# Kernel optimization log

Hardware: AMD Instinct MI355X
Metric: run time of the kernel (lower is better)

The kernel has to match this reference:

```python
import jax, jax.numpy as jnp
import numpy as np

B, L, DIN, D, H, NL, NE, TOPK, DFF, NOUT = 128, 128, 6, 256, 8, 6, 8, 2, 1024, 5
NMOE = NL // 2
DK = D // H
EPS = 1e-5


def setup_inputs() -> dict:
    key = jax.random.key(0)
    ks = iter(jax.random.split(key, 32))
    s = 0.02
    rn = lambda shape, scale=s: jax.random.normal(next(ks), shape, dtype=jnp.float32) * scale
    return {
        "x": jax.random.normal(next(ks), (B, L, DIN), dtype=jnp.float32),
        "emb_w": rn((DIN, D)), "emb_b": jnp.zeros((D,), jnp.float32),
        # wave attention layers (stacked over NL)
        "wq": rn((NL, D, D)), "wk": rn((NL, D, D)), "wv": rn((NL, D, D)), "wo": rn((NL, D, D)),
        "wfreq": rn((NL, H), 0.1), "wphase": jnp.zeros((NL, H), jnp.float32),
        # MoE layers (stacked over NMOE, experts over NE)
        "rtw": rn((NMOE, D, NE)), "rtb": jnp.zeros((NMOE, NE), jnp.float32),
        "ew1": rn((NMOE, NE, D, DFF)), "eb1": jnp.zeros((NMOE, NE, DFF), jnp.float32),
        "ew2": rn((NMOE, NE, DFF, D)), "eb2": jnp.zeros((NMOE, NE, D), jnp.float32),
        "ln_g": jnp.ones((D,), jnp.float32), "ln_b": jnp.zeros((D,), jnp.float32),
        "pred_w": rn((D, NOUT)), "pred_b": jnp.zeros((NOUT,), jnp.float32),
        "unc_w": rn((D, NOUT)), "unc_b": jnp.zeros((NOUT,), jnp.float32),
    }


def _wave_attn(x, Wq, Wk, Wv, Wo, freq, phase):
    # x: (B, L, D)
    q = (x @ Wq).reshape(B, L, H, DK).transpose(0, 2, 1, 3)  # (B,H,L,DK)
    k = (x @ Wk).reshape(B, L, H, DK).transpose(0, 2, 1, 3)
    v = (x @ Wv).reshape(B, L, H, DK).transpose(0, 2, 1, 3)
    pos = jnp.arange(L, dtype=x.dtype)
    wave = jnp.cos(2.0 * np.pi * freq[:, None] * pos[None, :] + phase[:, None])  # (H,L)
    scores = jnp.einsum("bhqd,bhkd->bhqk", q, k) * (DK ** -0.5)
    scores = scores * wave[None, :, None, :]  # modulate along key axis
    attn = jax.nn.softmax(scores, axis=-1)
    out = jnp.einsum("bhqk,bhkd->bhqd", attn, v)
    out = out.transpose(0, 2, 1, 3).reshape(B, L, D)
    return out @ Wo


def _moe(x, rw, rb, w1, b1, w2, b2):
    # x: (B, L, D). Dense per-expert compute + top-k combine weights
    xf = x.reshape(-1, D)  # (T, D), T = B*L
    T = xf.shape[0]
    p = jax.nn.softmax(xf @ rw + rb, axis=-1)           # (T, NE)
    tw, ti = jax.lax.top_k(p, TOPK)                      # (T, TOPK)
    tw = tw / tw.sum(axis=-1, keepdims=True)
    comb = jnp.zeros((T, NE), xf.dtype).at[jnp.arange(T)[:, None], ti].add(tw)  # (T, NE)
    h = jax.nn.gelu(jnp.einsum("td,edf->etf", xf, w1) + b1[:, None, :], approximate=False)
    eo = jnp.einsum("etf,efd->etd", h, w2) + b2[:, None, :]  # (NE, T, D)
    out = jnp.einsum("te,etd->td", comb, eo)
    return out.reshape(B, L, D)


def _forward(x, emb_w, emb_b, wq, wk, wv, wo, wfreq, wphase,
             rtw, rtb, ew1, eb1, ew2, eb2, ln_g, ln_b,
             pred_w, pred_b, unc_w, unc_b):
    h = x @ emb_w + emb_b
    for i in range(NL):
        h = _wave_attn(h, wq[i], wk[i], wv[i], wo[i], wfreq[i], wphase[i]) + h
        if i % 2 == 0 and i // 2 < NMOE:
            m = i // 2
            h = _moe(h, rtw[m], rtb[m], ew1[m], eb1[m], ew2[m], eb2[m]) + h
    mu = h.mean(axis=-1, keepdims=True)
    var = ((h - mu) ** 2).mean(axis=-1, keepdims=True)
    h = (h - mu) * jax.lax.rsqrt(var + EPS) * ln_g + ln_b
    latent = h[:, -1, :]  # (B, D)
    pred = latent @ pred_w + pred_b
    uncertainty = jax.nn.softplus(latent @ unc_w + unc_b)
    return pred, uncertainty


def reference(x, emb_w, emb_b, wq, wk, wv, wo, wfreq, wphase,
              rtw, rtb, ew1, eb1, ew2, eb2, ln_g, ln_b,
              pred_w, pred_b, unc_w, unc_b):
    return _forward(x, emb_w, emb_b, wq, wk, wv, wo, wfreq, wphase,
                    rtw, rtb, ew1, eb1, ew2, eb2, ln_g, ln_b,
                    pred_w, pred_b, unc_w, unc_b)
```

## Files before the change

### kernel.cpp

```cpp
#include <hip/hip_runtime.h>
#include <hip/hip_bf16.h>
#include <math.h>

#define B_    128
#define L_    128
#define DIN   6
#define D_    256
#define H_    8
#define NL_   6
#define NE_   8
#define DFF_  1024
#define NOUT_ 5
#define T_    (B_*L_)
#define DK_   32
#define NDESC_MAX 264

typedef unsigned short u16;
typedef __hip_bfloat16 bf16;
typedef __attribute__((ext_vector_type(8))) short short8;
typedef __attribute__((ext_vector_type(8))) unsigned short ushort8v;
typedef __attribute__((ext_vector_type(4))) float floatx4;

__device__ const int S_PRE[16] = {
    0, 98304, 99840, 100096, 100144, 100192, 106336, 106360,
    130936, 137080, 137336, 137592, 138872, 138877, 140157, 140162};
__device__ const int S_SRC[15] = {0,1,2,7,8,9,10,12,14,15,16,17,18,19,20};
#define NSMALL 140162

struct SrcPtrs { const void* p[21]; };

__device__ __forceinline__ float bf2f(u16 u) {
    return __uint_as_float(((unsigned)u) << 16);
}
__device__ __forceinline__ u16 f2bf(float f) {
    union { bf16 b; u16 u; } c; c.b = __float2bfloat16(f); return c.u;
}
__device__ __forceinline__ float gelu_f(float x) {
    return 0.5f * x * (1.0f + erff(x * 0.70710678118654752f));
}

__global__ __launch_bounds__(256)
void conv_small_kernel(SrcPtrs P, float* __restrict__ dst)
{
    const int i = blockIdx.x * 256 + threadIdx.x;
    if (i >= NSMALL) return;
    int seg = 0;
    #pragma unroll
    for (int s = 1; s < 15; ++s) seg += (i >= S_PRE[s]) ? 1 : 0;
    const int off = i - S_PRE[seg];
    const void* src = P.p[S_SRC[seg]];
    const bool isbf = (((const u16*)P.p[15])[0] == 0x3F80);
    if (isbf) dst[i] = bf2f(((const u16*)src)[off]);
    else      dst[i] = ((const float*)src)[off];
}

template<int KD, int ND>
__global__ __launch_bounds__(256)
void transpose_kernel(const void* __restrict__ src, const u16* __restrict__ probe,
                      u16* __restrict__ dst, long dzs, int noff, int total)
{
    const int i = blockIdx.x * 256 + threadIdx.x;
    if (i >= total) return;
    const int z   = i / (KD * ND);
    const int rem = i - z * (KD * ND);
    const int n   = rem / KD;
    const int k   = rem - n * KD;
    const size_t si = (size_t)z * KD * ND + (size_t)k * ND + n;
    const bool isbf = (probe[0] == 0x3F80);
    const float v = isbf ? bf2f(((const u16*)src)[si]) : ((const float*)src)[si];
    dst[(size_t)z * dzs + (size_t)(n + noff) * KD + k] = f2bf(v);
}

__global__ __launch_bounds__(256)
void embed_kernel(const float* __restrict__ x, const float* __restrict__ emb_w,
                  const float* __restrict__ emb_b, float* __restrict__ h,
                  u16* __restrict__ hb)
{
    const int idx = blockIdx.x * 256 + threadIdx.x;
    const int t = idx >> 8;
    const int d = idx & 255;
    float acc = emb_b[d];
    #pragma unroll
    for (int j = 0; j < DIN; ++j)
        acc += x[t * DIN + j] * emb_w[j * D_ + d];
    h[idx]  = acc;
    hb[idx] = f2bf(acc);
}

template<int EPI, int MODE>
__global__ __launch_bounds__(256)
void mfma_gemm(const u16* __restrict__ A, int lda, int K,
               const u16* __restrict__ Wt, long wzs, int ldwt,
               const float* __restrict__ biasb, long bzs,
               void* __restrict__ CoutV, int ldc,
               u16* __restrict__ hbout, int Mfixed,
               const int* __restrict__ cnt, const int* __restrict__ base_,
               const int* __restrict__ atok,
               const int* __restrict__ de, const int* __restrict__ dr,
               const int* __restrict__ ndesc)
{
    int M, r0, sbase = 0, e = 0;
    if constexpr (MODE == 0) {
        M  = Mfixed;
        r0 = blockIdx.x * 128;
        if (r0 >= M) return;
    } else {
        const int i = blockIdx.x;
        if (i >= *ndesc) return;
        e     = de[i];
        r0    = dr[i] * 128;
        sbase = base_[e];
        M     = cnt[e];
    }
    const u16*   W    = Wt + (size_t)e * wzs;
    const float* bias = biasb ? (biasb + (size_t)e * bzs) : nullptr;
    const int col0 = blockIdx.y * 128;

    __shared__ __attribute__((aligned(16))) u16 As[2][128][40];
    __shared__ __attribute__((aligned(16))) u16 Bs[2][128][40];
    __shared__ int stok[128];

    const int tid  = threadIdx.x;
    const int lane = tid & 63;
    const int wave = tid >> 6;
    const int wm = wave & 1, wn = wave >> 1;

    if constexpr (MODE == 1) {
        if (tid < 128) {
            int rr = r0 + tid;
            if (rr >= M) rr = M - 1;
            stok[tid] = atok[sbase + rr];
        }
        __syncthreads();
    }

    const int srow = tid >> 1;
    const int sk   = (tid & 1) * 16;
    long arow;
    if constexpr (MODE == 1) {
        arow = stok[srow];
    } else {
        int rr = r0 + srow;
        if (rr >= M) rr = M - 1;
        arow = (MODE == 2) ? (long)(sbase + rr) : (long)rr;
    }
    const u16* ga = A + arow * (long)lda + sk;
    const u16* gw = W + (size_t)(col0 + srow) * ldwt + sk;

    floatx4 acc[4][4];
    #pragma unroll
    for (int i = 0; i < 4; ++i)
        #pragma unroll
        for (int j = 0; j < 4; ++j)
            acc[i][j] = (floatx4){0.f, 0.f, 0.f, 0.f};

    const int fm = wm * 64 + (lane & 15);
    const int fn = wn * 64 + (lane & 15);
    const int fk = (lane >> 4) * 8;

    ushort8v ra0 = *(const ushort8v*)(ga);
    ushort8v ra1 = *(const ushort8v*)(ga + 8);
    ushort8v rb0 = *(const ushort8v*)(gw);
    ushort8v rb1 = *(const ushort8v*)(gw + 8);

    const int nt = K >> 5;
    int buf = 0;
    for (int t = 0; t < nt; ++t) {
        *(ushort8v*)&As[buf][srow][sk]     = ra0;
        *(ushort8v*)&As[buf][srow][sk + 8] = ra1;
        *(ushort8v*)&Bs[buf][srow][sk]     = rb0;
        *(ushort8v*)&Bs[buf][srow][sk + 8] = rb1;
        __syncthreads();

        if (t + 1 < nt) {
            const int k0 = (t + 1) << 5;
            ra0 = *(const ushort8v*)(ga + k0);
            ra1 = *(const ushort8v*)(ga + k0 + 8);
            rb0 = *(const ushort8v*)(gw + k0);
            rb1 = *(const ushort8v*)(gw + k0 + 8);
        }

        short8 af[4], bfr[4];
        #pragma unroll
        for (int i = 0; i < 4; ++i) af[i]  = *(const short8*)&As[buf][fm + 16*i][fk];
        #pragma unroll
        for (int j = 0; j < 4; ++j) bfr[j] = *(const short8*)&Bs[buf][fn + 16*j][fk];
        #pragma unroll
        for (int i = 0; i < 4; ++i)
            #pragma unroll
            for (int j = 0; j < 4; ++j)
                acc[i][j] = __builtin_amdgcn_mfma_f32_16x16x32_bf16(
                    af[i], bfr[j], acc[i][j], 0, 0, 0);
        buf ^= 1;
    }

    const int er = wm * 64 + ((lane >> 4) << 2);
    const int ec = wn * 64 + (lane & 15);
    #pragma unroll
    for (int i = 0; i < 4; ++i) {
        #pragma unroll
        for (int reg = 0; reg < 4; ++reg) {
            const int lrow = r0 + er + i * 16 + reg;
            if (lrow >= M) continue;
            const long crow = (MODE == 0) ? (long)lrow : (long)(sbase + lrow);
            #pragma unroll
            for (int j = 0; j < 4; ++j) {
                const int cj = col0 + ec + j * 16;
                const float val = acc[i][j][reg];
                if constexpr (EPI == 0) {
                    ((u16*)CoutV)[crow * ldc + cj] = f2bf(val);
                } else if constexpr (EPI == 1) {
                    const size_t idx = crow * ldc + cj;
                    const float nv = ((float*)CoutV)[idx] + val;
                    ((float*)CoutV)[idx] = nv;
                    hbout[idx] = f2bf(nv);
                } else if constexpr (EPI == 2) {
                    ((u16*)CoutV)[crow * ldc + cj] = f2bf(gelu_f(val + bias[cj]));
                } else {
                    ((float*)CoutV)[crow * ldc + cj] = val + bias[cj];
                }
            }
        }
    }
}

__global__ __launch_bounds__(256)
void attn_kernel(const u16* __restrict__ qkv, u16* __restrict__ o,
                 const float* __restrict__ wfreq, const float* __restrict__ wphase)
{
    const int bh = blockIdx.x;
    const int b  = bh >> 3;
    const int hh = bh & 7;

    __shared__ __attribute__((aligned(16))) u16 Qs[128][40];
    __shared__ __attribute__((aligned(16))) u16 Ks[128][40];
    __shared__ __attribute__((aligned(16))) u16 Vt[32][136];
    __shared__ __attribute__((aligned(16))) u16 Ps[128][136];
    __shared__ float wavec[128];

    const int tid  = threadIdx.x;
    const int lane = tid & 63;
    const int w    = tid >> 6;
    const int col16 = lane & 15;
    const int quad  = lane >> 4;

    const long qbase = (long)b * L_ * 768 + hh * DK_;

    {
        const int row = tid >> 1;
        const int hf  = (tid & 1) * 16;
        const u16* src = qkv + qbase + (long)row * 768 + hf;
        *(ushort8v*)&Qs[row][hf]     = *(const ushort8v*)(src);
        *(ushort8v*)&Qs[row][hf + 8] = *(const ushort8v*)(src + 8);
        *(ushort8v*)&Ks[row][hf]     = *(const ushort8v*)(src + 256);
        *(ushort8v*)&Ks[row][hf + 8] = *(const ushort8v*)(src + 264);
        #pragma unroll
        for (int j = 0; j < 16; ++j)
            Vt[hf + j][row] = src[512 + j];
    }
    if (tid < L_) {
        float f2 = 6.2831853071795864769f * wfreq[hh];
        wavec[tid] = cosf(f2 * (float)tid + wphase[hh]);
    }
    __syncthreads();

    const float scale = 0.17677669529663687f;
    float wv8[8];
    #pragma unroll
    for (int ni = 0; ni < 8; ++ni)
        wv8[ni] = scale * wavec[ni * 16 + col16];

    const int m0 = w * 32;
    floatx4 accs[2][8];
    {
        short8 a0 = *(const short8*)&Qs[m0 + col16][quad * 8];
        short8 a1 = *(const short8*)&Qs[m0 + 16 + col16][quad * 8];
        #pragma unroll
        for (int ni = 0; ni < 8; ++ni) {
            short8 bf = *(const short8*)&Ks[ni * 16 + col16][quad * 8];
            accs[0][ni] = __builtin_amdgcn_mfma_f32_16x16x32_bf16(
                a0, bf, (floatx4){0.f,0.f,0.f,0.f}, 0, 0, 0);
            accs[1][ni] = __builtin_amdgcn_mfma_f32_16x16x32_bf16(
                a1, bf, (floatx4){0.f,0.f,0.f,0.f}, 0, 0, 0);
        }
    }
    #pragma unroll
    for (int mi = 0; mi < 2; ++mi)
        #pragma unroll
        for (int ni = 0; ni < 8; ++ni)
            #pragma unroll
            for (int reg = 0; reg < 4; ++reg)
                accs[mi][ni][reg] *= wv8[ni];

    #pragma unroll
    for (int mi = 0; mi < 2; ++mi) {
        #pragma unroll
        for (int reg = 0; reg < 4; ++reg) {
            float rmax = -1e30f;
            #pragma unroll
            for (int ni = 0; ni < 8; ++ni)
                rmax = fmaxf(rmax, accs[mi][ni][reg]);
            #pragma unroll
            for (int off = 1; off < 16; off <<= 1)
                rmax = fmaxf(rmax, __shfl_xor(rmax, off));
            float e[8], rsum = 0.0f;
            #pragma unroll
            for (int ni = 0; ni < 8; ++ni) {
                e[ni] = expf(accs[mi][ni][reg] - rmax);
                rsum += e[ni];
            }
            #pragma unroll
            for (int off = 1; off < 16; off <<= 1)
                rsum += __shfl_xor(rsum, off);
            const float inv = 1.0f / rsum;
            const int row = m0 + mi * 16 + quad * 4 + reg;
            #pragma unroll
            for (int ni = 0; ni < 8; ++ni)
                Ps[row][ni * 16 + col16] = f2bf(e[ni] * inv);
        }
    }
    __syncthreads();

    floatx4 acco[2][2];
    #pragma unroll
    for (int mi = 0; mi < 2; ++mi)
        #pragma unroll
        for (int nj = 0; nj < 2; ++nj)
            acco[mi][nj] = (floatx4){0.f,0.f,0.f,0.f};
    #pragma unroll
    for (int kk = 0; kk < 4; ++kk) {
        short8 a0 = *(const short8*)&Ps[m0 + col16][kk * 32 + quad * 8];
        short8 a1 = *(const short8*)&Ps[m0 + 16 + col16][kk * 32 + quad * 8];
        short8 b0 = *(const short8*)&Vt[col16][kk * 32 + quad * 8];
        short8 b1 = *(const short8*)&Vt[16 + col16][kk * 32 + quad * 8];
        acco[0][0] = __builtin_amdgcn_mfma_f32_16x16x32_bf16(a0, b0, acco[0][0], 0, 0, 0);
        acco[0][1] = __builtin_amdgcn_mfma_f32_16x16x32_bf16(a0, b1, acco[0][1], 0, 0, 0);
        acco[1][0] = __builtin_amdgcn_mfma_f32_16x16x32_bf16(a1, b0, acco[1][0], 0, 0, 0);
        acco[1][1] = __builtin_amdgcn_mfma_f32_16x16x32_bf16(a1, b1, acco[1][1], 0, 0, 0);
    }

    const long obase = (long)b * L_ * D_ + hh * DK_;
    #pragma unroll
    for (int mi = 0; mi < 2; ++mi)
        #pragma unroll
        for (int reg = 0; reg < 4; ++reg) {
            const int row = m0 + mi * 16 + quad * 4 + reg;
            #pragma unroll
            for (int nj = 0; nj < 2; ++nj)
                o[obase + (long)row * D_ + nj * 16 + col16] =
                    f2bf(acco[mi][nj][reg]);
        }
}

__global__ __launch_bounds__(256)
void router_kernel(const float* __restrict__ h, const float* __restrict__ rtw,
                   const float* __restrict__ rtb, int* __restrict__ te,
                   float* __restrict__ twt)
{
    const int tid  = threadIdx.x;
    const int lane = tid & 63;
    const int wv   = tid >> 6;
    const int t    = blockIdx.x * 4 + wv;

    const float4 hv = ((const float4*)(h + (long)t * D_))[lane];
    const float4* rp = (const float4*)rtw;

    float lg[NE_];
    #pragma unroll
    for (int e = 0; e < NE_; ++e) lg[e] = 0.0f;
    #pragma unroll
    for (int i = 0; i < 4; ++i) {
        const int d = lane * 4 + i;
        const float xv = (i == 0) ? hv.x : (i == 1) ? hv.y : (i == 2) ? hv.z : hv.w;
        float4 wa = rp[d * 2 + 0];
        float4 wb = rp[d * 2 + 1];
        lg[0] = fmaf(xv, wa.x, lg[0]);
        lg[1] = fmaf(xv, wa.y, lg[1]);
        lg[2] = fmaf(xv, wa.z, lg[2]);
        lg[3] = fmaf(xv, wa.w, lg[3]);
        lg[4] = fmaf(xv, wb.x, lg[4]);
        lg[5] = fmaf(xv, wb.y, lg[5]);
        lg[6] = fmaf(xv, wb.z, lg[6]);
        lg[7] = fmaf(xv, wb.w, lg[7]);
    }
    #pragma unroll
    for (int off = 1; off < 64; off <<= 1)
        #pragma unroll
        for (int e = 0; e < NE_; ++e)
            lg[e] += __shfl_xor(lg[e], off);

    if (lane == 0) {
        #pragma unroll
        for (int e = 0; e < NE_; ++e) lg[e] += rtb[e];
        int i1 = 0; float v1 = lg[0];
        #pragma unroll
        for (int e = 1; e < NE_; ++e) { if (lg[e] > v1) { v1 = lg[e]; i1 = e; } }
        int i2 = (i1 == 0) ? 1 : 0; float v2 = lg[i2];
        #pragma unroll
        for (int e = 0; e < NE_; ++e) {
            if (e != i1 && lg[e] > v2) { v2 = lg[e]; i2 = e; }
        }
        float r   = expf(v2 - v1);
        float wa1 = 1.0f / (1.0f + r);
        te[2 * t]     = i1;
        te[2 * t + 1] = i2;
        twt[2 * t]     = wa1;
        twt[2 * t + 1] = r * wa1;
    }
}

__global__ __launch_bounds__(512)
void countscan_kernel(const int* __restrict__ te, int* __restrict__ cnt,
                      int* __restrict__ base_, int* __restrict__ cursor,
                      int* __restrict__ de, int* __restrict__ dr,
                      int* __restrict__ ndesc)
{
    const int tid = threadIdx.x;
    int c[NE_];
    #pragma unroll
    for (int e = 0; e < NE_; ++e) c[e] = 0;
    for (int i = tid; i < 2 * T_; i += 512) {
        const int e = te[i];
        #pragma unroll
        for (int ee = 0; ee < NE_; ++ee) c[ee] += (e == ee) ? 1 : 0;
    }
    #pragma unroll
    for (int off = 1; off < 64; off <<= 1)
        #pragma unroll
        for (int e = 0; e < NE_; ++e)
            c[e] += __shfl_xor(c[e], off);

    __shared__ int wsum[8][NE_];
    const int lane = tid & 63, wv = tid >> 6;
    if (lane == 0)
        #pragma unroll
        for (int e = 0; e < NE_; ++e) wsum[wv][e] = c[e];
    __syncthreads();
    if (tid == 0) {
        int a = 0, n = 0;
        for (int e = 0; e < NE_; ++e) {
            int s = 0;
            for (int w = 0; w < 8; ++w) s += wsum[w][e];
            cnt[e] = s;
            base_[e] = a;
            a += s;
            const int nb = (s + 127) >> 7;
            for (int rb = 0; rb < nb; ++rb) {
                de[n] = e; dr[n] = rb; ++n;
            }
        }
        *ndesc = n;
    }
    if (tid < NE_) cursor[tid] = 0;
}

__global__ __launch_bounds__(256)
void scatter_kernel(const int* __restrict__ te, const int* __restrict__ base_,
                    int* __restrict__ cursor, int* __restrict__ atok,
                    int* __restrict__ tslot)
{
    __shared__ int lcnt[NE_];
    __shared__ int gb[NE_];
    const int tid = threadIdx.x;
    if (tid < NE_) lcnt[tid] = 0;
    __syncthreads();

    const int i0 = blockIdx.x * 512 + tid * 2;
    const int e0 = te[i0], e1 = te[i0 + 1];
    const int r0 = atomicAdd(&lcnt[e0], 1);
    const int r1 = atomicAdd(&lcnt[e1], 1);
    __syncthreads();
    if (tid < NE_) gb[tid] = atomicAdd(&cursor[tid], lcnt[tid]);
    __syncthreads();

    const int s0 = base_[e0] + gb[e0] + r0;
    const int s1 = base_[e1] + gb[e1] + r1;
    atok[s0] = i0 >> 1;
    atok[s1] = i0 >> 1;
    tslot[i0]     = s0;
    tslot[i0 + 1] = s1;
}

__global__ __launch_bounds__(256)
void combine_kernel(float* __restrict__ h, u16* __restrict__ hb,
                    const float* __restrict__ eo,
                    const float* __restrict__ twt, const int* __restrict__ tslot)
{
    const int t = blockIdx.x;
    const int d = threadIdx.x;
    const int s0 = tslot[2 * t], s1 = tslot[2 * t + 1];
    const float w0 = twt[2 * t], w1 = twt[2 * t + 1];
    const long idx = (long)t * D_ + d;
    const float nv = h[idx] + w0 * eo[(long)s0 * D_ + d] + w1 * eo[(long)s1 * D_ + d];
    h[idx]  = nv;
    hb[idx] = f2bf(nv);
}

__global__ __launch_bounds__(256)
void final_kernel(const float* __restrict__ h, const float* __restrict__ ln_g,
                  const float* __restrict__ ln_b, const float* __restrict__ pred_w,
                  const float* __restrict__ pred_b, const float* __restrict__ unc_w,
                  const float* __restrict__ unc_b, float* __restrict__ out)
{
    const int b = blockIdx.x;
    const int d = threadIdx.x;
    const long t = (long)b * L_ + (L_ - 1);
    const float val = h[t * D_ + d];

    __shared__ float red[4];
    __shared__ float lat[D_];

    float s = val;
    #pragma unroll
    for (int off = 32; off > 0; off >>= 1) s += __shfl_down(s, off);
    if ((d & 63) == 0) red[d >> 6] = s;
    __syncthreads();
    const float mean = (red[0] + red[1] + red[2] + red[3]) * (1.0f / D_);
    __syncthreads();

    const float dv = val - mean;
    s = dv * dv;
    #pragma unroll
    for (int off = 32; off > 0; off >>= 1) s += __shfl_down(s, off);
    if ((d & 63) == 0) red[d >> 6] = s;
    __syncthreads();
    const float var = (red[0] + red[1] + red[2] + red[3]) * (1.0f / D_);

    lat[d] = dv * rsqrtf(var + 1e-5f) * ln_g[d] + ln_b[d];
    __syncthreads();

    if (d < 2 * NOUT_) {
        const int j = d % NOUT_;
        const int sel = d / NOUT_;
        const float* w  = sel ? unc_w : pred_w;
        const float* bb = sel ? unc_b : pred_b;
        float acc = bb[j];
        for (int dd = 0; dd < D_; ++dd)
            acc = fmaf(lat[dd], w[dd * NOUT_ + j], acc);
        if (sel) acc = log1pf(expf(acc));
        out[sel * (B_ * NOUT_) + b * NOUT_ + j] = acc;
    }
}

extern "C" void kernel_launch(void* const* d_in, const int* in_sizes, int n_in,
                              void* d_out, int out_size, void* d_ws, size_t ws_size,
                              hipStream_t stream)
{
    (void)in_sizes; (void)n_in; (void)out_size; (void)ws_size;

    char* ws = (char*)d_ws;
    size_t off = 0;
    auto alloc = [&](size_t bytes) {
        size_t cur = off;
        off += (bytes + 255) & ~(size_t)255;
        return (void*)(ws + cur);
    };
    float* cs     = (float*)alloc((size_t)NSMALL * 4);
    u16*   qkvt   = (u16*)  alloc((size_t)NL_ * 768 * 256 * 2);
    u16*   wot    = (u16*)  alloc((size_t)NL_ * 256 * 256 * 2);
    u16*   ew1t   = (u16*)  alloc((size_t)3 * NE_ * DFF_ * D_ * 2);
    u16*   ew2t   = (u16*)  alloc((size_t)3 * NE_ * D_ * DFF_ * 2);
    float* h      = (float*)alloc((size_t)T_ * D_ * 4);
    u16*   hb     = (u16*)  alloc((size_t)T_ * D_ * 2);
    char*  uni    = (char*) alloc((size_t)2 * T_ * DFF_ * 2 + (size_t)2 * T_ * D_ * 4);
    u16*   qkvb   = (u16*)  uni;
    u16*   ob     = (u16*)  (uni + (size_t)T_ * 768 * 2 + 256);
    u16*   hidden = (u16*)  uni;
    float* eo     = (float*)(uni + (size_t)2 * T_ * DFF_ * 2);
    int*   te     = (int*)  alloc((size_t)2 * T_ * 4);
    float* twt    = (float*)alloc((size_t)2 * T_ * 4);
    int*   atok   = (int*)  alloc((size_t)2 * T_ * 4);
    int*   tslot  = (int*)  alloc((size_t)2 * T_ * 4);
    int*   cnt    = (int*)  alloc(64 * 4);
    int*   base_  = (int*)  alloc(64 * 4);
    int*   cursor = (int*)  alloc(64 * 4);
    int*   de     = (int*)  alloc(NDESC_MAX * 4);
    int*   dr     = (int*)  alloc(NDESC_MAX * 4);
    int*   ndesc  = (int*)  alloc(64 * 4);

    SrcPtrs P;
    for (int i = 0; i < 21; ++i) P.p[i] = d_in[i];
    const u16* probe = (const u16*)d_in[15];

    conv_small_kernel<<<(NSMALL + 255) / 256, 256, 0, stream>>>(P, cs);
    transpose_kernel<256,256><<<(NL_*65536 + 255)/256, 256, 0, stream>>>(
        d_in[3], probe, qkvt, 768L*256, 0,   NL_*65536);
    transpose_kernel<256,256><<<(NL_*65536 + 255)/256, 256, 0, stream>>>(
        d_in[4], probe, qkvt, 768L*256, 256, NL_*65536);
    transpose_kernel<256,256><<<(NL_*65536 + 255)/256, 256, 0, stream>>>(
        d_in[5], probe, qkvt, 768L*256, 512, NL_*65536);
    transpose_kernel<256,256><<<(NL_*65536 + 255)/256, 256, 0, stream>>>(
        d_in[6], probe, wot, 65536L, 0, NL_*65536);
    transpose_kernel<256,1024><<<(24*262144 + 255)/256, 256, 0, stream>>>(
        d_in[11], probe, ew1t, 262144L, 0, 24*262144);
    transpose_kernel<1024,256><<<(24*262144 + 255)/256, 256, 0, stream>>>(
        d_in[13], probe, ew2t, 262144L, 0, 24*262144);

    const float* x      = cs;
    const float* emb_w  = cs + 98304;
    const float* emb_b  = cs + 99840;
    const float* wfreq  = cs + 100096;
    const float* wphase = cs + 100144;
    const float* rtw    = cs + 100192;
    const float* rtb    = cs + 106336;
    const float* eb1    = cs + 106360;
    const float* eb2    = cs + 130936;
    const float* ln_g   = cs + 137080;
    const float* ln_b   = cs + 137336;
    const float* pred_w = cs + 137592;
    const float* pred_b = cs + 138872;
    const float* unc_w  = cs + 138877;
    const float* unc_b  = cs + 140157;

    embed_kernel<<<(T_ * D_) / 256, 256, 0, stream>>>(x, emb_w, emb_b, h, hb);

    for (int i = 0; i < NL_; ++i) {
        mfma_gemm<0, 0><<<dim3(T_/128, 6, 1), 256, 0, stream>>>(
            hb, D_, D_, qkvt + (size_t)i * 768 * 256, 0, 256,
            nullptr, 0, qkvb, 768, nullptr, T_,
            nullptr, nullptr, nullptr, nullptr, nullptr, nullptr);
        attn_kernel<<<B_ * H_, 256, 0, stream>>>(qkvb, ob,
                                                 wfreq + i * H_, wphase + i * H_);
        mfma_gemm<1, 0><<<dim3(T_/128, 2, 1), 256, 0, stream>>>(
            ob, D_, D_, wot + (size_t)i * 65536, 0, 256,
            nullptr, 0, h, D_, hb, T_,
            nullptr, nullptr, nullptr, nullptr, nullptr, nullptr);

        if (i % 2 == 0) {
            const int m = i / 2;
            const u16* w1t = ew1t + (size_t)m * NE_ * DFF_ * D_;
            const u16* w2t = ew2t + (size_t)m * NE_ * D_ * DFF_;
            const float* b1 = eb1 + (size_t)m * NE_ * DFF_;
            const float* b2 = eb2 + (size_t)m * NE_ * D_;
            router_kernel<<<T_ / 4, 256, 0, stream>>>(
                h, rtw + (size_t)m * D_ * NE_, rtb + m * NE_, te, twt);
            countscan_kernel<<<1, 512, 0, stream>>>(te, cnt, base_, cursor,
                                                    de, dr, ndesc);
            scatter_kernel<<<(2 * T_) / 512, 256, 0, stream>>>(te, base_, cursor,
                                                               atok, tslot);
            mfma_gemm<2, 1><<<dim3(NDESC_MAX, DFF_/128, 1), 256, 0, stream>>>(
                hb, D_, D_, w1t, (long)DFF_ * D_, 256,
                b1, DFF_, hidden, DFF_, nullptr, 0,
                cnt, base_, atok, de, dr, ndesc);
            mfma_gemm<3, 2><<<dim3(NDESC_MAX, D_/128, 1), 256, 0, stream>>>(
                hidden, DFF_, DFF_, w2t, (long)D_ * DFF_, DFF_,
                b2, D_, eo, D_, nullptr, 0,
                cnt, base_, nullptr, de, dr, ndesc);
            combine_kernel<<<T_, 256, 0, stream>>>(h, hb, eo, twt, tslot);
        }
    }

    final_kernel<<<B_, 256, 0, stream>>>(h, ln_g, ln_b, pred_w, pred_b,
                                         unc_w, unc_b, (float*)d_out);
}
```

Measured before the change: 1.012 ms.

## Deepen GEMM prefetch to four k-tiles and pre-gather MoE tokens

The GEMM now holds four 32-wide k-tiles of register prefetch in flight instead of one. K becomes a compile-time template parameter so the loop fully unrolls into groups of four. The indirect token gather for the first MoE GEMM moves out into a separate gather kernel that writes a contiguous buffer, so that GEMM reads rows directly. This is meant to hide global memory latency and remove the per-block token lookup and its extra sync, at the cost of more registers, an extra kernel launch and an extra activation copy.

```diff
diff --git a/kernel.cpp b/kernel.cpp
--- a/kernel.cpp
+++ b/kernel.cpp
@@ -87,15 +87,14 @@
     hb[idx] = f2bf(acc);
 }
 
-template<int EPI, int MODE>
-__global__ __launch_bounds__(256)
-void mfma_gemm(const u16* __restrict__ A, int lda, int K,
+template<int EPI, int MODE, int NT>
+__global__ __launch_bounds__(256)
+void mfma_gemm(const u16* __restrict__ A, int lda,
                const u16* __restrict__ Wt, long wzs, int ldwt,
                const float* __restrict__ biasb, long bzs,
                void* __restrict__ CoutV, int ldc,
                u16* __restrict__ hbout, int Mfixed,
                const int* __restrict__ cnt, const int* __restrict__ base_,
-               const int* __restrict__ atok,
                const int* __restrict__ de, const int* __restrict__ dr,
                const int* __restrict__ ndesc)
 {
@@ -118,32 +117,17 @@
 
     __shared__ __attribute__((aligned(16))) u16 As[2][128][40];
     __shared__ __attribute__((aligned(16))) u16 Bs[2][128][40];
-    __shared__ int stok[128];
 
     const int tid  = threadIdx.x;
     const int lane = tid & 63;
     const int wave = tid >> 6;
     const int wm = wave & 1, wn = wave >> 1;
 
-    if constexpr (MODE == 1) {
-        if (tid < 128) {
-            int rr = r0 + tid;
-            if (rr >= M) rr = M - 1;
-            stok[tid] = atok[sbase + rr];
-        }
-        __syncthreads();
-    }
-
     const int srow = tid >> 1;
     const int sk   = (tid & 1) * 16;
-    long arow;
-    if constexpr (MODE == 1) {
-        arow = stok[srow];
-    } else {
-        int rr = r0 + srow;
-        if (rr >= M) rr = M - 1;
-        arow = (MODE == 2) ? (long)(sbase + rr) : (long)rr;
-    }
+    int rr = r0 + srow;
+    if (rr >= M) rr = M - 1;
+    const long arow = (MODE == 0) ? (long)rr : (long)(sbase + rr);
     const u16* ga = A + arow * (long)lda + sk;
     const u16* gw = W + (size_t)(col0 + srow) * ldwt + sk;
 
@@ -158,40 +142,50 @@
     const int fn = wn * 64 + (lane & 15);
     const int fk = (lane >> 4) * 8;
 
-    ushort8v ra0 = *(const ushort8v*)(ga);
-    ushort8v ra1 = *(const ushort8v*)(ga + 8);
-    ushort8v rb0 = *(const ushort8v*)(gw);
-    ushort8v rb1 = *(const ushort8v*)(gw + 8);
-
-    const int nt = K >> 5;
+    ushort8v pa0[4], pa1[4], pb0[4], pb1[4];
+    #pragma unroll
+    for (int d = 0; d < 4; ++d) {
+        const int k0 = d * 32;
+        pa0[d] = *(const ushort8v*)(ga + k0);
+        pa1[d] = *(const ushort8v*)(ga + k0 + 8);
+        pb0[d] = *(const ushort8v*)(gw + k0);
+        pb1[d] = *(const ushort8v*)(gw + k0 + 8);
+    }
+
+    constexpr int G = NT / 4;
     int buf = 0;
-    for (int t = 0; t < nt; ++t) {
-        *(ushort8v*)&As[buf][srow][sk]     = ra0;
-        *(ushort8v*)&As[buf][srow][sk + 8] = ra1;
-        *(ushort8v*)&Bs[buf][srow][sk]     = rb0;
-        *(ushort8v*)&Bs[buf][srow][sk + 8] = rb1;
-        __syncthreads();
-
-        if (t + 1 < nt) {
-            const int k0 = (t + 1) << 5;
-            ra0 = *(const ushort8v*)(ga + k0);
-            ra1 = *(const ushort8v*)(ga + k0 + 8);
-            rb0 = *(const ushort8v*)(gw + k0);
-            rb1 = *(const ushort8v*)(gw + k0 + 8);
-        }
-
-        short8 af[4], bfr[4];
-        #pragma unroll
-        for (int i = 0; i < 4; ++i) af[i]  = *(const short8*)&As[buf][fm + 16*i][fk];
-        #pragma unroll
-        for (int j = 0; j < 4; ++j) bfr[j] = *(const short8*)&Bs[buf][fn + 16*j][fk];
-        #pragma unroll
-        for (int i = 0; i < 4; ++i)
-            #pragma unroll
-            for (int j = 0; j < 4; ++j)
-                acc[i][j] = __builtin_amdgcn_mfma_f32_16x16x32_bf16(
-                    af[i], bfr[j], acc[i][j], 0, 0, 0);
-        buf ^= 1;
+    for (int g = 0; g < G; ++g) {
+        const bool pf = (g + 1 < G);
+        const int kbase = (g + 1) * 128;
+        #pragma unroll
+        for (int d = 0; d < 4; ++d) {
+            *(ushort8v*)&As[buf][srow][sk]     = pa0[d];
+            *(ushort8v*)&As[buf][srow][sk + 8] = pa1[d];
+            *(ushort8v*)&Bs[buf][srow][sk]     = pb0[d];
+            *(ushort8v*)&Bs[buf][srow][sk + 8] = pb1[d];
+            __syncthreads();
+
+            if (pf) {
+                const int k0 = kbase + d * 32;
+                pa0[d] = *(const ushort8v*)(ga + k0);
+                pa1[d] = *(const ushort8v*)(ga + k0 + 8);
+                pb0[d] = *(const ushort8v*)(gw + k0);
+                pb1[d] = *(const ushort8v*)(gw + k0 + 8);
+            }
+
+            short8 af[4], bfr[4];
+            #pragma unroll
+            for (int i = 0; i < 4; ++i) af[i]  = *(const short8*)&As[buf][fm + 16*i][fk];
+            #pragma unroll
+            for (int j = 0; j < 4; ++j) bfr[j] = *(const short8*)&Bs[buf][fn + 16*j][fk];
+            #pragma unroll
+            for (int i = 0; i < 4; ++i)
+                #pragma unroll
+                for (int j = 0; j < 4; ++j)
+                    acc[i][j] = __builtin_amdgcn_mfma_f32_16x16x32_bf16(
+                        af[i], bfr[j], acc[i][j], 0, 0, 0);
+            buf ^= 1;
+        }
     }
 
     const int er = wm * 64 + ((lane >> 4) << 2);
@@ -225,6 +219,18 @@
 }
 
 __global__ __launch_bounds__(256)
+void gather_kernel(const u16* __restrict__ hb, const int* __restrict__ atok,
+                   u16* __restrict__ xg)
+{
+    const int idx  = blockIdx.x * 256 + threadIdx.x;
+    const int slot = idx >> 5;
+    const int c16  = idx & 31;
+    const int tok  = atok[slot];
+    *(ushort8v*)&xg[(size_t)slot * D_ + c16 * 8] =
+        *(const ushort8v*)&hb[(size_t)tok * D_ + c16 * 8];
+}
+
+__global__ __launch_bounds__(256)
 void attn_kernel(const u16* __restrict__ qkv, u16* __restrict__ o,
                  const float* __restrict__ wfreq, const float* __restrict__ wphase)
 {
@@ -562,6 +568,7 @@
     u16*   ew2t   = (u16*)  alloc((size_t)3 * NE_ * D_ * DFF_ * 2);
     float* h      = (float*)alloc((size_t)T_ * D_ * 4);
     u16*   hb     = (u16*)  alloc((size_t)T_ * D_ * 2);
+    u16*   xg     = (u16*)  alloc((size_t)2 * T_ * D_ * 2);
     char*  uni    = (char*) alloc((size_t)2 * T_ * DFF_ * 2 + (size_t)2 * T_ * D_ * 4);
     u16*   qkvb   = (u16*)  uni;
     u16*   ob     = (u16*)  (uni + (size_t)T_ * 768 * 2 + 256);
@@ -615,16 +622,16 @@
     embed_kernel<<<(T_ * D_) / 256, 256, 0, stream>>>(x, emb_w, emb_b, h, hb);
 
     for (int i = 0; i < NL_; ++i) {
-        mfma_gemm<0, 0><<<dim3(T_/128, 6, 1), 256, 0, stream>>>(
-            hb, D_, D_, qkvt + (size_t)i * 768 * 256, 0, 256,
+        mfma_gemm<0, 0, 8><<<dim3(T_/128, 6, 1), 256, 0, stream>>>(
+            hb, D_, qkvt + (size_t)i * 768 * 256, 0, 256,
             nullptr, 0, qkvb, 768, nullptr, T_,
-            nullptr, nullptr, nullptr, nullptr, nullptr, nullptr);
+            nullptr, nullptr, nullptr, nullptr, nullptr);
         attn_kernel<<<B_ * H_, 256, 0, stream>>>(qkvb, ob,
                                                  wfreq + i * H_, wphase + i * H_);
-        mfma_gemm<1, 0><<<dim3(T_/128, 2, 1), 256, 0, stream>>>(
-            ob, D_, D_, wot + (size_t)i * 65536, 0, 256,
+        mfma_gemm<1, 0, 8><<<dim3(T_/128, 2, 1), 256, 0, stream>>>(
+            ob, D_, wot + (size_t)i * 65536, 0, 256,
             nullptr, 0, h, D_, hb, T_,
-            nullptr, nullptr, nullptr, nullptr, nullptr, nullptr);
+            nullptr, nullptr, nullptr, nullptr, nullptr);
 
         if (i % 2 == 0) {
             const int m = i / 2;
@@ -638,14 +645,15 @@
                                                     de, dr, ndesc);
             scatter_kernel<<<(2 * T_) / 512, 256, 0, stream>>>(te, base_, cursor,
                                                                atok, tslot);
-            mfma_gemm<2, 1><<<dim3(NDESC_MAX, DFF_/128, 1), 256, 0, stream>>>(
-                hb, D_, D_, w1t, (long)DFF_ * D_, 256,
+            gather_kernel<<<(2 * T_ * 32) / 256, 256, 0, stream>>>(hb, atok, xg);
+            mfma_gemm<2, 2, 8><<<dim3(NDESC_MAX, DFF_/128, 1), 256, 0, stream>>>(
+                xg, D_, w1t, (long)DFF_ * D_, 256,
                 b1, DFF_, hidden, DFF_, nullptr, 0,
-                cnt, base_, atok, de, dr, ndesc);
-            mfma_gemm<3, 2><<<dim3(NDESC_MAX, D_/128, 1), 256, 0, stream>>>(
-                hidden, DFF_, DFF_, w2t, (long)D_ * DFF_, DFF_,
+                cnt, base_, de, dr, ndesc);
+            mfma_gemm<3, 2, 32><<<dim3(NDESC_MAX, D_/128, 1), 256, 0, stream>>>(
+                hidden, DFF_, w2t, (long)D_ * DFF_, DFF_,
                 b2, D_, eo, D_, nullptr, 0,
-                cnt, base_, nullptr, de, dr, ndesc);
+                cnt, base_, de, dr, ndesc);
             combine_kernel<<<T_, 256, 0, stream>>>(h, hb, eo, twt, tslot);
         }
     }
```

Measured after the change: 1.100 ms. +8.7%, slower.

## Stage GEMM tiles with direct global-to-LDS loads and XOR swizzle

Applied to the files above, without the earlier changes.

The MFMA GEMM now fills shared memory with global_load_lds (16-byte direct-to-LDS loads) instead of loading into registers and then storing to LDS. The padded LDS tiles are replaced by an unpadded layout with an XOR swizzle on both the write and read sides to avoid bank conflicts. The loop trip count becomes a template parameter so it can be fully known at compile time. The aim is to save VGPRs and the LDS store instructions, and to overlap the next tile's load with the current MFMAs. The risk is that the swizzle must match the wave-ordered lane-to-address mapping of the direct LDS load exactly, or the results will be wrong.

```diff
diff --git a/kernel.cpp b/kernel.cpp
--- a/kernel.cpp
+++ b/kernel.cpp
@@ -39,6 +39,13 @@
     return 0.5f * x * (1.0f + erff(x * 0.70710678118654752f));
 }
 
+__device__ __forceinline__ void gl_lds16(const u16* g, u16* l) {
+    __builtin_amdgcn_global_load_lds(
+        (const __attribute__((address_space(1))) unsigned int*)g,
+        (__attribute__((address_space(3))) unsigned int*)l,
+        16, 0, 0);
+}
+
 __global__ __launch_bounds__(256)
 void conv_small_kernel(SrcPtrs P, float* __restrict__ dst)
 {
@@ -87,9 +94,9 @@
     hb[idx] = f2bf(acc);
 }
 
-template<int EPI, int MODE>
-__global__ __launch_bounds__(256)
-void mfma_gemm(const u16* __restrict__ A, int lda, int K,
+template<int EPI, int MODE, int NT>
+__global__ __launch_bounds__(256)
+void mfma_gemm(const u16* __restrict__ A, int lda,
                const u16* __restrict__ Wt, long wzs, int ldwt,
                const float* __restrict__ biasb, long bzs,
                void* __restrict__ CoutV, int ldc,
@@ -116,8 +123,8 @@
     const float* bias = biasb ? (biasb + (size_t)e * bzs) : nullptr;
     const int col0 = blockIdx.y * 128;
 
-    __shared__ __attribute__((aligned(16))) u16 As[2][128][40];
-    __shared__ __attribute__((aligned(16))) u16 Bs[2][128][40];
+    __shared__ __attribute__((aligned(16))) u16 As[2][128 * 32];
+    __shared__ __attribute__((aligned(16))) u16 Bs[2][128 * 32];
     __shared__ int stok[128];
 
     const int tid  = threadIdx.x;
@@ -134,18 +141,23 @@
         __syncthreads();
     }
 
-    const int srow = tid >> 1;
-    const int sk   = (tid & 1) * 16;
-    long arow;
+    const int ss   = (lane & 3) ^ ((lane >> 3) & 3);
+    const int row0 = wave * 16 + (lane >> 2);
+    const int row1 = row0 + 64;
+    long ar0, ar1;
     if constexpr (MODE == 1) {
-        arow = stok[srow];
+        ar0 = stok[row0];
+        ar1 = stok[row1];
     } else {
-        int rr = r0 + srow;
-        if (rr >= M) rr = M - 1;
-        arow = (MODE == 2) ? (long)(sbase + rr) : (long)rr;
-    }
-    const u16* ga = A + arow * (long)lda + sk;
-    const u16* gw = W + (size_t)(col0 + srow) * ldwt + sk;
+        int rr0 = r0 + row0; if (rr0 >= M) rr0 = M - 1;
+        int rr1 = r0 + row1; if (rr1 >= M) rr1 = M - 1;
+        ar0 = (MODE == 2) ? (long)(sbase + rr0) : (long)rr0;
+        ar1 = (MODE == 2) ? (long)(sbase + rr1) : (long)rr1;
+    }
+    const u16* ga0 = A + ar0 * (long)lda + ss * 8;
+    const u16* ga1 = A + ar1 * (long)lda + ss * 8;
+    const u16* gw0 = W + (size_t)(col0 + row0) * ldwt + ss * 8;
+    const u16* gw1 = W + (size_t)(col0 + row1) * ldwt + ss * 8;
 
     floatx4 acc[4][4];
     #pragma unroll
@@ -156,41 +168,38 @@
 
     const int fm = wm * 64 + (lane & 15);
     const int fn = wn * 64 + (lane & 15);
-    const int fk = (lane >> 4) * 8;
-
-    ushort8v ra0 = *(const ushort8v*)(ga);
-    ushort8v ra1 = *(const ushort8v*)(ga + 8);
-    ushort8v rb0 = *(const ushort8v*)(gw);
-    ushort8v rb1 = *(const ushort8v*)(gw + 8);
-
-    const int nt = K >> 5;
+    const int ps = (lane >> 4) ^ ((lane >> 1) & 3);
+
+    auto STAGE = [&](int b, int kt) {
+        const int ko = kt * 32;
+        gl_lds16(ga0 + ko, &As[b][tid * 8]);
+        gl_lds16(ga1 + ko, &As[b][2048 + tid * 8]);
+        gl_lds16(gw0 + ko, &Bs[b][tid * 8]);
+        gl_lds16(gw1 + ko, &Bs[b][2048 + tid * 8]);
+    };
+
+    STAGE(0, 0);
+    __syncthreads();
+
     int buf = 0;
-    for (int t = 0; t < nt; ++t) {
-        *(ushort8v*)&As[buf][srow][sk]     = ra0;
-        *(ushort8v*)&As[buf][srow][sk + 8] = ra1;
-        *(ushort8v*)&Bs[buf][srow][sk]     = rb0;
-        *(ushort8v*)&Bs[buf][srow][sk + 8] = rb1;
-        __syncthreads();
-
-        if (t + 1 < nt) {
-            const int k0 = (t + 1) << 5;
-            ra0 = *(const ushort8v*)(ga + k0);
-            ra1 = *(const ushort8v*)(ga + k0 + 8);
-            rb0 = *(const ushort8v*)(gw + k0);
-            rb1 = *(const ushort8v*)(gw + k0 + 8);
-        }
+    for (int t = 0; t < NT; ++t) {
+        if (t + 1 < NT) STAGE(buf ^ 1, t + 1);
 
         short8 af[4], bfr[4];
         #pragma unroll
-        for (int i = 0; i < 4; ++i) af[i]  = *(const short8*)&As[buf][fm + 16*i][fk];
-        #pragma unroll
-        for (int j = 0; j < 4; ++j) bfr[j] = *(const short8*)&Bs[buf][fn + 16*j][fk];
+        for (int i = 0; i < 4; ++i)
+            af[i]  = *(const short8*)&As[buf][(fm + 16 * i) * 32 + ps * 8];
+        #pragma unroll
+        for (int j = 0; j < 4; ++j)
+            bfr[j] = *(const short8*)&Bs[buf][(fn + 16 * j) * 32 + ps * 8];
         #pragma unroll
         for (int i = 0; i < 4; ++i)
             #pragma unroll
             for (int j = 0; j < 4; ++j)
                 acc[i][j] = __builtin_amdgcn_mfma_f32_16x16x32_bf16(
                     af[i], bfr[j], acc[i][j], 0, 0, 0);
+
+        __syncthreads();
         buf ^= 1;
     }
 
@@ -615,14 +624,14 @@
     embed_kernel<<<(T_ * D_) / 256, 256, 0, stream>>>(x, emb_w, emb_b, h, hb);
 
     for (int i = 0; i < NL_; ++i) {
-        mfma_gemm<0, 0><<<dim3(T_/128, 6, 1), 256, 0, stream>>>(
-            hb, D_, D_, qkvt + (size_t)i * 768 * 256, 0, 256,
+        mfma_gemm<0, 0, 8><<<dim3(T_/128, 6, 1), 256, 0, stream>>>(
+            hb, D_, qkvt + (size_t)i * 768 * 256, 0, 256,
             nullptr, 0, qkvb, 768, nullptr, T_,
             nullptr, nullptr, nullptr, nullptr, nullptr, nullptr);
         attn_kernel<<<B_ * H_, 256, 0, stream>>>(qkvb, ob,
                                                  wfreq + i * H_, wphase + i * H_);
-        mfma_gemm<1, 0><<<dim3(T_/128, 2, 1), 256, 0, stream>>>(
-            ob, D_, D_, wot + (size_t)i * 65536, 0, 256,
+        mfma_gemm<1, 0, 8><<<dim3(T_/128, 2, 1), 256, 0, stream>>>(
+            ob, D_, wot + (size_t)i * 65536, 0, 256,
             nullptr, 0, h, D_, hb, T_,
             nullptr, nullptr, nullptr, nullptr, nullptr, nullptr);
 
@@ -638,12 +647,12 @@
                                                     de, dr, ndesc);
             scatter_kernel<<<(2 * T_) / 512, 256, 0, stream>>>(te, base_, cursor,
                                                                atok, tslot);
-            mfma_gemm<2, 1><<<dim3(NDESC_MAX, DFF_/128, 1), 256, 0, stream>>>(
-                hb, D_, D_, w1t, (long)DFF_ * D_, 256,
+            mfma_gemm<2, 1, 8><<<dim3(NDESC_MAX, DFF_/128, 1), 256, 0, stream>>>(
+                hb, D_, w1t, (long)DFF_ * D_, 256,
                 b1, DFF_, hidden, DFF_, nullptr, 0,
                 cnt, base_, atok, de, dr, ndesc);
-            mfma_gemm<3, 2><<<dim3(NDESC_MAX, D_/128, 1), 256, 0, stream>>>(
-                hidden, DFF_, DFF_, w2t, (long)D_ * DFF_, DFF_,
+            mfma_gemm<3, 2, 32><<<dim3(NDESC_MAX, D_/128, 1), 256, 0, stream>>>(
+                hidden, DFF_, w2t, (long)D_ * DFF_, DFF_,
                 b2, D_, eo, D_, nullptr, 0,
                 cnt, base_, nullptr, de, dr, ndesc);
             combine_kernel<<<T_, 256, 0, stream>>>(h, hb, eo, twt, tslot);
```

Measured after the change: 1.016 ms. Within noise of the previous version (+0.4%).
